# Kernel optimization log

Measured on AMD Instinct MI355X. Metric: run time of the kernel, lower is better.

## Reference

```python
import jax, jax.numpy as jnp
import numpy as np

B, H, W = 8, 128, 128
WIDTH, MODES = 32, 12
NL = 6


def _spectral_conv(x, w):
    # x: [B,C,H,W] real; w: [2, Cin, Cout, m, m, 2] (real/imag packed)
    b, c, h, ww = x.shape
    m = w.shape[3]
    xf = jnp.fft.rfft2(x)  # [B,C,H,W//2+1] complex
    w1 = w[0, ..., 0] + 1j * w[0, ..., 1]
    w2 = w[1, ..., 0] + 1j * w[1, ..., 1]
    top = jnp.einsum('bixy,ioxy->boxy', xf[:, :, :m, :m], w1)
    bot = jnp.einsum('bixy,ioxy->boxy', xf[:, :, -m:, :m], w2)
    out = jnp.zeros((b, w.shape[2], h, ww // 2 + 1), dtype=xf.dtype)
    out = out.at[:, :, :m, :m].set(top).at[:, :, -m:, :m].set(bot)
    return jnp.fft.irfft2(out, s=(h, ww))


def _conv1x1(x, wgt, bia):
    # x: [B,C,H,W], wgt: [O,C], bia: [O]
    return jnp.einsum('bchw,oc->bohw', x, wgt) + bia[None, :, None, None]


def _gelu(x):
    return jax.nn.gelu(x, approximate=False)


def setup_inputs() -> dict:
    key = jax.random.key(0)
    ks = jax.random.split(key, 20)
    scale = 1.0 / (WIDTH * WIDTH)
    d = {}
    d['x'] = jax.random.normal(ks[0], (B, H, W, 4), jnp.float32)
    d['fc0_W'] = jax.random.normal(ks[1], (4, WIDTH), jnp.float32) * 0.5
    d['fc0_b'] = jnp.zeros((WIDTH,), jnp.float32)
    d['spec_w'] = scale * jax.random.uniform(ks[2], (NL, 2, WIDTH, WIDTH, MODES, MODES, 2), jnp.float32)
    d['wW'] = jax.random.normal(ks[3], (NL, WIDTH, WIDTH), jnp.float32) * (1.0 / np.sqrt(WIDTH))
    d['wb'] = jnp.zeros((NL, WIDTH), jnp.float32)
    d['bW'] = jax.random.normal(ks[4], (NL, WIDTH, 2), jnp.float32) * 0.7
    d['bb'] = jnp.zeros((NL, WIDTH), jnp.float32)
    d['cW'] = jax.random.normal(ks[5], (NL, WIDTH, 3), jnp.float32) * 0.57
    d['cb'] = jnp.zeros((NL, WIDTH), jnp.float32)
    d['fc1_W'] = jax.random.normal(ks[6], (WIDTH, 256), jnp.float32) * (1.0 / np.sqrt(WIDTH))
    d['fc1_b'] = jnp.zeros((256,), jnp.float32)
    d['fc3_W'] = jax.random.normal(ks[7], (256, 128), jnp.float32) * (1.0 / 16.0)
    d['fc3_b'] = jnp.zeros((128,), jnp.float32)
    d['fc4_W'] = jax.random.normal(ks[8], (128, 128), jnp.float32) * (1.0 / np.sqrt(128.0))
    d['fc4_b'] = jnp.zeros((128,), jnp.float32)
    d['fc5_W'] = jax.random.normal(ks[9], (128, 1), jnp.float32) * (1.0 / np.sqrt(128.0))
    d['fc5_b'] = jnp.zeros((1,), jnp.float32)
    return d


def reference(x, fc0_W, fc0_b, spec_w, wW, wb, bW, bb, cW, cb,
              fc1_W, fc1_b, fc3_W, fc3_b, fc4_W, fc4_b, fc5_W, fc5_b):
    b, h, w, _ = x.shape
    grid_mesh = jnp.transpose(x[:, :, :, 1:4], (0, 3, 1, 2))  # [B,3,H,W]
    y = x @ fc0_W + fc0_b                                     # [B,H,W,width]
    y = jnp.transpose(y, (0, 3, 1, 2))                        # [B,width,H,W]
    gx = jnp.linspace(0.0, 1.0, h, dtype=jnp.float32)
    gy = jnp.linspace(0.0, 1.0, w, dtype=jnp.float32)
    grid = jnp.stack([
        jnp.broadcast_to(gx[:, None], (h, w)),
        jnp.broadcast_to(gy[None, :], (h, w)),
    ], axis=0)                                                # [2,H,W]
    grid = jnp.broadcast_to(grid[None], (b, 2, h, w))
    for l in range(NL):
        y = _gelu(_spectral_conv(y, spec_w[l])
                  + _conv1x1(y, wW[l], wb[l])
                  + _conv1x1(grid, bW[l], bb[l])
                  + _conv1x1(grid_mesh, cW[l], cb[l]))
    y = jnp.transpose(y, (0, 2, 3, 1))                        # [B,H,W,width]
    y = _gelu(y @ fc1_W + fc1_b)
    y = _gelu(y @ fc3_W + fc3_b)
    y = y @ fc4_W + fc4_b
    y = y @ fc5_W + fc5_b
    return y
```

## Files before the change

### kernel.cpp

```cpp
#include <hip/hip_runtime.h>
#include <math.h>


#define NL 6

typedef unsigned short u16;
typedef __attribute__((ext_vector_type(8))) short short8v;
typedef __attribute__((ext_vector_type(8))) unsigned short ushort8v;
typedef __attribute__((ext_vector_type(4))) unsigned short ushort4v;
typedef __attribute__((ext_vector_type(4))) float f32x4;

__device__ __forceinline__ float gelu_f(float x){
  float z  = x*0.70710678118654752f;
  float az = fabsf(z);
  float t  = __builtin_amdgcn_rcpf(fmaf(0.3275911f, az, 1.0f));
  float p  = t*(0.254829592f + t*(-0.284496736f + t*(1.421413741f +
             t*(-1.453152027f + t*1.061405429f))));
  float e  = __expf(-z*z);
  float er = copysignf(fmaf(-p, e, 1.0f), z);
  return 0.5f*x*(1.0f + er);
}
__device__ __forceinline__ u16 f2bf(float x){
  unsigned u = __float_as_uint(x);
  u += 0x7FFF + ((u>>16)&1);
  return (u16)(u>>16);
}
__device__ __forceinline__ float bf2f(u16 h){
  return __uint_as_float(((unsigned)h)<<16);
}
__device__ __forceinline__ void split2(float v, u16 &hh, u16 &ll){
  unsigned u = __float_as_uint(v);
  hh = (u16)(u>>16);
  float lo = v - __uint_as_float(u & 0xFFFF0000u);
  ll = (u16)(__float_as_uint(lo)>>16);
}

__global__ __launch_bounds__(256) void k_fc0f(const float* __restrict__ x,
                      const float* __restrict__ W, const float* __restrict__ b,
                      float* __restrict__ y, float* __restrict__ F1){
  __shared__ float Ws[128];
  __shared__ float bs[32];
  __shared__ float ys2[2][32][132];
  int t = threadIdx.x;
  if (t < 128) Ws[t] = W[t];
  if (t < 32)  bs[t] = b[t];
  __syncthreads();
  int pix = blockIdx.x*256 + t;
  float4 xv = *reinterpret_cast<const float4*>(x + (size_t)pix*4);
  int bb = pix >> 14, hw = pix & 16383;
  int r = t>>7, w = t&127;
  float* yp = y + (size_t)bb*32*16384 + hw;
  #pragma unroll
  for (int c=0;c<32;c++){
    float acc = bs[c] + xv.x*Ws[c] + xv.y*Ws[32+c] + xv.z*Ws[64+c] + xv.w*Ws[96+c];
    yp[(size_t)c*16384] = acc;
    ys2[r][c][w] = acc;
  }
  __syncthreads();
  int c2 = t>>3, wq = t&7;
  float stc[12], sts[12];
  #pragma unroll
  for (int k=0;k<12;k++){ float s,c; sincospif(k*(1.0f/64.0f), &s, &c); stc[k]=c; sts[k]=s; }
  int gr0 = blockIdx.x*2;
  #pragma unroll
  for (int r2=0;r2<2;r2++){
    float cr[12], ci[12], aR[12], aI[12];
    #pragma unroll
    for (int k=0;k<12;k++){
      float s,c; sincospif((float)(k*wq)*0.25f, &s, &c);
      cr[k]=c; ci[k]=s; aR[k]=0.f; aI[k]=0.f;
    }
    const float* rowp = &ys2[r2][c2][wq*16];
    #pragma unroll
    for (int q=0;q<4;q++){
      float4 xq = *reinterpret_cast<const float4*>(rowp + q*4);
      float xa[4]={xq.x,xq.y,xq.z,xq.w};
      #pragma unroll
      for (int e=0;e<4;e++){
        float xw = xa[e];
        #pragma unroll
        for (int k=0;k<12;k++){
          aR[k] += xw*cr[k];
          aI[k] -= xw*ci[k];
          float nc = cr[k]*stc[k] - ci[k]*sts[k];
          ci[k]    = cr[k]*sts[k] + ci[k]*stc[k];
          cr[k] = nc;
        }
      }
    }
    #pragma unroll
    for (int k=0;k<12;k++){
      aR[k] += __shfl_xor(aR[k],1); aR[k] += __shfl_xor(aR[k],2); aR[k] += __shfl_xor(aR[k],4);
      aI[k] += __shfl_xor(aI[k],1); aI[k] += __shfl_xor(aI[k],2); aI[k] += __shfl_xor(aI[k],4);
    }
    if (wq==0){
      int g = gr0 + r2; int b2 = g>>7, h2 = g&127;
      float* dst = F1 + ((size_t)(b2*32+c2)*128 + h2)*24;
      #pragma unroll
      for (int k=0;k<12;k++){ dst[2*k] = aR[k]; dst[2*k+1] = aI[k]; }
    }
  }
}

__global__ __launch_bounds__(256) void k_wtrans(const float* __restrict__ w, float* __restrict__ wT){
  __shared__ float buf[16][32][25];
  int t=threadIdx.x;
  int beta = blockIdx.x;
  int l = beta/48, r = beta%48;
  int hf = r/24; int r2 = r%24;
  int kym = r2>>1; int i0 = (r2&1)*16;
  const float* src = w + (size_t)l*589824 + (size_t)hf*294912 + kym*24;
  float* dst = wT + (size_t)l*589824 + (size_t)hf*294912 + (size_t)kym*24576;
  for (int j=t; j<12288; j+=256){
    int i = j/768, rem = j%768, o = rem/24, kxri = rem%24;
    buf[i][o][kxri] = src[(size_t)(i0+i)*9216 + o*288 + kxri];
  }
  __syncthreads();
  for (int j=t; j<12288; j+=256){
    int kx = j>>10, rem = j&1023, i = rem>>6, orr = rem&63, o = orr>>1, ri = orr&1;
    dst[(size_t)kx*2048 + o*64 + (i0+i)*2 + ri] = buf[i][o][kx*2+ri];
  }
}

__global__ __launch_bounds__(256) void k_wprep(const float* __restrict__ W1, const float* __restrict__ W3,
                       const float* __restrict__ W4,
                       const float* __restrict__ b4, const float* __restrict__ w5,
                       const float* __restrict__ b5,
                       u16* __restrict__ W1h, u16* __restrict__ W1l,
                       u16* __restrict__ W3h, u16* __restrict__ W3l,
                       u16* __restrict__ W4h, u16* __restrict__ W4l,
                       u16* __restrict__ Emh, u16* __restrict__ Eml,
                       u16* __restrict__ E2h, u16* __restrict__ E2l,
                       u16* __restrict__ E3h, u16* __restrict__ E3l,
                       float* __restrict__ c45){
  __shared__ float buf[32][132];
  int t = threadIdx.x, bid = blockIdx.x;
  if (bid < 8){
    int k0 = bid*32;
    for (int i=t;i<4096;i+=256){ int k=i>>7, n=i&127; buf[k][n] = W3[(size_t)(k0+k)*128 + n]; }
    __syncthreads();
    int n = t>>1, kq = t&1;
    #pragma unroll
    for (int kk=0;kk<16;kk++){
      int k = kq*16 + kk;
      float v = buf[k][n];
      u16 hh = f2bf(v);
      W3h[(size_t)bid*4096 + n*32 + k] = hh;
      W3l[(size_t)bid*4096 + n*32 + k] = f2bf(v - bf2f(hh));
    }
  } else if (bid == 8){
    __shared__ float red[256];
    int n = t;
    #pragma unroll
    for (int c=0;c<32;c++){
      float v = W1[(size_t)c*256 + n];
      u16 hh = f2bf(v);
      W1h[n*32 + c] = hh;
      W1l[n*32 + c] = f2bf(v - bf2f(hh));
    }
    red[t] = (t<128)? b4[t]*w5[t] : 0.f;
    __syncthreads();
    for (int s2=128; s2>0; s2>>=1){
      if (t<s2) red[t] += red[t+s2];
      __syncthreads();
    }
    if (t==0) c45[0] = red[0] + b5[0];
  } else if (bid <= 12){
    int k0 = (bid-9)*32;
    for (int i=t;i<4096;i+=256){ int k=i>>7, n=i&127; buf[k][n] = W4[(size_t)(k0+k)*128 + n]; }
    __syncthreads();
    int n = t>>1, kq = t&1;
    #pragma unroll
    for (int kk=0;kk<16;kk++){
      int k = kq*16 + kk;
      float v = buf[k][n];
      u16 hh = f2bf(v);
      W4h[(size_t)(bid-9)*4096 + n*32 + k] = hh;
      W4l[(size_t)(bid-9)*4096 + n*32 + k] = f2bf(v - bf2f(hh));
    }
  } else if (bid == 13){
    for (int i=t;i<4096;i+=256){
      int m=i>>7, w=i&127;
      float v=0.f;
      if (m<24){ float s,c; sincospif((float)((m>>1)*w)*(1.0f/64.0f), &s, &c); v = (m&1)? -s : c; }
      u16 hh, ll; split2(v, hh, ll);
      Emh[i]=hh; Eml[i]=ll;
    }
  } else if (bid == 14){
    for (int i=t;i<12288;i+=256){
      int m=i>>8, k=i&255;
      int kyi = (m<24)? m : m-24;
      int ky  = (kyi<12)? kyi : kyi+104;
      int h   = k&127;
      int mm  = (ky*h)&127;
      float s,c; sincospif((float)mm*(1.0f/64.0f), &s, &c);
      bool sinSlot = k>=128;
      float v;
      if (m<24) v = sinSlot? s : c;
      else      v = sinSlot? c : -s;
      u16 hh, ll; split2(v, hh, ll);
      E2h[i]=hh; E2l[i]=ll;
    }
  } else {
    for (int i=t;i<8192;i+=256){
      int h=i>>6, k=i&63;
      float v=0.f;
      if (k<48){
        int kyi = (k<24)? k : k-24;
        int ky  = (kyi<12)? kyi : kyi+104;
        int mm  = (ky*h)&127;
        float s,c; sincospif((float)mm*(1.0f/64.0f), &s, &c);
        v = ((k<24)? c : s) * (1.0f/16384.0f);
      }
      u16 hh, ll; split2(v, hh, ll);
      E3h[i]=hh; E3l[i]=ll;
    }
  }
}

__global__ __launch_bounds__(256) void k_dfth(const float* __restrict__ F1,
                      const u16* __restrict__ E2h, const u16* __restrict__ E2l,
                      float* __restrict__ F2){
  __shared__ u16 Fth[16*264], Ftl[16*264];
  int t=threadIdx.x;
  int bc = blockIdx.x;
  int b = bc>>5, c = bc&31;
  const float* src = F1 + (size_t)bc*3072;
  for (int i=t;i<3072;i+=256){
    int h = i/24, col = i - h*24;
    int kx = col>>1, ri = col&1;
    u16 hh, ll; split2(src[i], hh, ll);
    int idx = kx*264 + ri*128 + h;
    Fth[idx] = hh; Ftl[idx] = ll;
  }
  __syncthreads();
  int wv = t>>6, lane = t&63, lr = lane&15, lg = lane>>4;
  if (wv < 3){
    f32x4 acc = (f32x4){0.f,0.f,0.f,0.f};
    #pragma unroll
    for (int ks=0; ks<8; ++ks){
      short8v af = *reinterpret_cast<const short8v*>(E2h + (size_t)(wv*16+lr)*256 + ks*32 + lg*8);
      short8v ag = *reinterpret_cast<const short8v*>(E2l + (size_t)(wv*16+lr)*256 + ks*32 + lg*8);
      short8v bf = *reinterpret_cast<const short8v*>(&Fth[lr*264 + ks*32 + lg*8]);
      short8v bg = *reinterpret_cast<const short8v*>(&Ftl[lr*264 + ks*32 + lg*8]);
      acc = __builtin_amdgcn_mfma_f32_16x16x32_bf16(af, bf, acc, 0,0,0);
      acc = __builtin_amdgcn_mfma_f32_16x16x32_bf16(af, bg, acc, 0,0,0);
      acc = __builtin_amdgcn_mfma_f32_16x16x32_bf16(ag, bf, acc, 0,0,0);
    }
    if (lr < 12){
      #pragma unroll
      for (int r=0;r<4;r++){
        int m = wv*16 + 4*lg + r;
        int kyi = (m<24)? m : m-24;
        int ri  = (m<24)? 0 : 1;
        F2[(((size_t)b*24 + kyi)*24 + 2*lr + ri)*32 + c] = acc[r];
      }
    }
  }
}

__global__ __launch_bounds__(576) void k_mixid(const float* __restrict__ F2, const float* __restrict__ wTl,
                      const u16* __restrict__ E3h, const u16* __restrict__ E3l,
                      float* __restrict__ S1){
  __shared__ u16 Bh[32*72], Bl[32*72];
  int t=threadIdx.x;
  int bo = blockIdx.x;
  int b = bo>>5, o = bo&31;
  for (int i=t; i<24*24; i+=576){
    int row = i/24, k = 48 + i - (i/24)*24;
    Bh[row*72 + k] = 0; Bl[row*72 + k] = 0;
  }
  {
    int pair = t>>1, half = t&1;
    int kx = pair%12, kyi = pair/12;
    int hf = kyi<12?0:1, kym = kyi<12?kyi:kyi-12;
    const float* fpr = F2 + (((size_t)b*24 + kyi)*24 + 2*kx)*32 + half*16;
    const float* fpi = fpr + 32;
    const float* wp = wTl + (size_t)(hf*12+kym)*24576 + kx*2048 + o*64 + half*32;
    float gr=0.f, gi=0.f;
    #pragma unroll 8
    for (int i=0;i<16;i++){
      float2 wv = *reinterpret_cast<const float2*>(wp + 2*i);
      float ar = fpr[i], ai = fpi[i];
      gr += ar*wv.x - ai*wv.y;
      gi += ar*wv.y + ai*wv.x;
    }
    gr += __shfl_xor(gr,1);
    gi += __shfl_xor(gi,1);
    if (half==0){
      u16 grh, grl, gih, gil, nih, nil;
      split2(gr, grh, grl);
      split2(gi, gih, gil);
      split2(-gi, nih, nil);
      int r0 = (2*kx)*72, r1 = (2*kx+1)*72;
      Bh[r0 + kyi]      = grh; Bl[r0 + kyi]      = grl;
      Bh[r0 + 24 + kyi] = nih; Bl[r0 + 24 + kyi] = nil;
      Bh[r1 + kyi]      = gih; Bl[r1 + kyi]      = gil;
      Bh[r1 + 24 + kyi] = grh; Bl[r1 + 24 + kyi] = grl;
    }
  }
  __syncthreads();
  int wv = t>>6, lane = t&63, lr = lane&15, lg = lane>>4;
  if (wv < 8){
    f32x4 acc[2];
    acc[0] = (f32x4){0.f,0.f,0.f,0.f};
    acc[1] = (f32x4){0.f,0.f,0.f,0.f};
    #pragma unroll
    for (int ks=0; ks<2; ++ks){
      short8v af = *reinterpret_cast<const short8v*>(E3h + (size_t)(wv*16+lr)*64 + ks*32 + lg*8);
      short8v ag = *reinterpret_cast<const short8v*>(E3l + (size_t)(wv*16+lr)*64 + ks*32 + lg*8);
      #pragma unroll
      for (int nt=0; nt<2; ++nt){
        short8v bf = *reinterpret_cast<const short8v*>(&Bh[(nt*16+lr)*72 + ks*32 + lg*8]);
        short8v bg = *reinterpret_cast<const short8v*>(&Bl[(nt*16+lr)*72 + ks*32 + lg*8]);
        acc[nt] = __builtin_amdgcn_mfma_f32_16x16x32_bf16(af, bf, acc[nt], 0,0,0);
        acc[nt] = __builtin_amdgcn_mfma_f32_16x16x32_bf16(af, bg, acc[nt], 0,0,0);
        acc[nt] = __builtin_amdgcn_mfma_f32_16x16x32_bf16(ag, bf, acc[nt], 0,0,0);
      }
    }
    float* dst = S1 + (size_t)bo*3072;
    #pragma unroll
    for (int nt=0; nt<2; ++nt){
      int n = nt*16 + lr;
      if (n < 24){
        #pragma unroll
        for (int r=0;r<4;r++){
          int h = wv*16 + 4*lg + r;
          dst[h*24 + n] = acc[nt][r];
        }
      }
    }
  }
}

template<int LAST>
__global__ __launch_bounds__(512) void k_combine2(const float* __restrict__ yin, const float* __restrict__ S1,
                         const float* __restrict__ x,
                         const float* __restrict__ wWl, const float* __restrict__ wbl,
                         const float* __restrict__ bWl, const float* __restrict__ bbl,
                         const float* __restrict__ cWl, const float* __restrict__ cbl,
                         const u16* __restrict__ Emh, const u16* __restrict__ Eml,
                         float* __restrict__ yout, float* __restrict__ F1,
                         u16* __restrict__ yb16){
  __shared__ float ysT[128][33];
  __shared__ u16 ybsp[2][32][136];
  int t=threadIdx.x;
  int b = blockIdx.x>>7, h = blockIdx.x&127;
  for (int i=t;i<4096;i+=512){ int c=i>>7, w=i&127;
    ysT[w][c] = yin[(((size_t)(b*32+c))*128+h)*128+w]; }
  __syncthreads();
  int w = t&127;
  int og = __builtin_amdgcn_readfirstlane(t>>7);
  float ct[12], st[12];
  ct[0]=1.f; st[0]=0.f;
  float c1,s1v; sincospif(w*(1.0f/64.0f), &s1v, &c1);
  #pragma unroll
  for (int k=0;k<11;k++){ ct[k+1] = ct[k]*c1 - st[k]*s1v; st[k+1] = ct[k]*s1v + st[k]*c1; }
  float gx = h*(1.0f/127.0f), gy = w*(1.0f/127.0f);
  float4 xm = *reinterpret_cast<const float4*>(x + (((size_t)(b*128+h))*128+w)*4);
  float m1=xm.y, m2=xm.z, m3=xm.w;
  const float* wo  = wWl + og*256;
  const float* s1o = S1 + (size_t)b*98304 + (size_t)og*8*3072 + h*24;
  float accv[8];
  #pragma unroll
  for (int oi=0;oi<8;oi++){
    int o = og*8+oi;
    float bse = wbl[o] + bbl[o] + cbl[o] + gx*bWl[o*2] + gy*bWl[o*2+1]
              + m1*cWl[o*3] + m2*cWl[o*3+1] + m3*cWl[o*3+2];
    const float* sp = s1o + (size_t)oi*3072;
    float spec = sp[0];
    #pragma unroll
    for (int kx=1;kx<12;kx++) spec += 2.0f*(sp[2*kx]*ct[kx] - sp[2*kx+1]*st[kx]);
    accv[oi] = bse + spec;
  }
  #pragma unroll
  for (int c=0;c<32;c++){
    float xc = ysT[w][c];
    #pragma unroll
    for (int oi=0;oi<8;oi++) accv[oi] += wo[oi*32+c]*xc;
  }
  #pragma unroll
  for (int oi=0;oi<8;oi++){
    float g = gelu_f(accv[oi]);
    int o = og*8+oi;
    if constexpr (!LAST){
      u16 hh, ll; split2(g, hh, ll);
      ybsp[0][o][w] = hh;
      ybsp[1][o][w] = ll;
      yout[(((size_t)(b*32+o))*128+h)*128+w] = g;
    } else {
      ybsp[0][o][w] = f2bf(g);
    }
  }
  __syncthreads();
  if constexpr (!LAST){
    int wv = t>>6;
    if (wv < 4){
      int lane = t&63, lr = lane&15, lg = lane>>4;
      int mt = wv&1, oj = wv>>1;
      f32x4 acc = (f32x4){0.f,0.f,0.f,0.f};
      #pragma unroll
      for (int ks=0; ks<4; ++ks){
        short8v ef = *reinterpret_cast<const short8v*>(Emh + (size_t)(mt*16+lr)*128 + ks*32 + lg*8);
        short8v eg = *reinterpret_cast<const short8v*>(Eml + (size_t)(mt*16+lr)*128 + ks*32 + lg*8);
        short8v yf = *reinterpret_cast<const short8v*>(&ybsp[0][oj*16+lr][ks*32+lg*8]);
        short8v yg = *reinterpret_cast<const short8v*>(&ybsp[1][oj*16+lr][ks*32+lg*8]);
        acc = __builtin_amdgcn_mfma_f32_16x16x32_bf16(ef, yf, acc, 0,0,0);
        acc = __builtin_amdgcn_mfma_f32_16x16x32_bf16(ef, yg, acc, 0,0,0);
        acc = __builtin_amdgcn_mfma_f32_16x16x32_bf16(eg, yf, acc, 0,0,0);
      }
      if (mt==0 || lg<2){
        int m = mt*16 + 4*lg;
        int o = oj*16 + lr;
        float4 v; v.x=acc[0]; v.y=acc[1]; v.z=acc[2]; v.w=acc[3];
        *reinterpret_cast<float4*>(&F1[((size_t)(b*32+o)*128 + h)*24 + m]) = v;
      }
    }
  } else {
    int wr = t>>2, hf4 = t&3;
    size_t pix = (size_t)b*16384 + h*128 + wr;
    ushort8v h8;
    #pragma unroll
    for (int q=0;q<8;q++) h8[q] = ybsp[0][hf4*8 + q][wr];
    *reinterpret_cast<ushort8v*>(yb16 + pix*32 + hf4*8) = h8;
  }
}

__global__ __launch_bounds__(256) void k_headm(
    const u16* __restrict__ Yb,
    const u16* __restrict__ W1h, const u16* __restrict__ W1l,
    const float* __restrict__ b1,
    const u16* __restrict__ W3h, const u16* __restrict__ W3l,
    const float* __restrict__ b3,
    const u16* __restrict__ W4h, const u16* __restrict__ W4l,
    const float* __restrict__ c45, const float* __restrict__ w5,
    float* __restrict__ out){
  __shared__ u16 Ac[64*264];
  __shared__ float b1s[256];
  __shared__ float b3s[128], w5s[128];
  __shared__ float part2[2][64];
  int t = threadIdx.x;
  int wv = t>>6, lane = t&63, lr = lane&15, lg = lane>>4;
  int P0 = blockIdx.x*64;
  b1s[t] = b1[t];
  if (t<128){ b3s[t]=b3[t]; w5s[t]=w5[t]; }
  int wn3 = wv>>1, wp = wv&1;
  short8v yb;
  {
    size_t p = (size_t)P0 + wv*16 + lr;
    yb = *reinterpret_cast<const short8v*>(Yb + p*32 + lg*8);
  }
  __syncthreads();

  unsigned q[8][2][2];
  #pragma unroll
  for (int kt=0; kt<8; ++kt){
    f32x4 a1[2];
    a1[0]=(f32x4){0,0,0,0}; a1[1]=(f32x4){0,0,0,0};
    #pragma unroll
    for (int i=0;i<2;i++){
      int n1 = kt*32 + i*16 + lr;
      short8v w1f = *reinterpret_cast<const short8v*>(W1h + (size_t)n1*32 + lg*8);
      short8v w1g = *reinterpret_cast<const short8v*>(W1l + (size_t)n1*32 + lg*8);
      a1[i] = __builtin_amdgcn_mfma_f32_16x16x32_bf16(w1f, yb, a1[i], 0,0,0);
      a1[i] = __builtin_amdgcn_mfma_f32_16x16x32_bf16(w1g, yb, a1[i], 0,0,0);
    }
    #pragma unroll
    for (int i=0;i<2;i++){
      int n1b = kt*32 + i*16 + 4*lg;
      u16 v0 = f2bf(gelu_f(a1[i][0] + b1s[n1b+0]));
      u16 v1 = f2bf(gelu_f(a1[i][1] + b1s[n1b+1]));
      u16 v2 = f2bf(gelu_f(a1[i][2] + b1s[n1b+2]));
      u16 v3 = f2bf(gelu_f(a1[i][3] + b1s[n1b+3]));
      q[kt][i][0] = (unsigned)v0 | ((unsigned)v1<<16);
      q[kt][i][1] = (unsigned)v2 | ((unsigned)v3<<16);
    }
  }
  {
    int p = wv*16 + lr;
    #pragma unroll
    for (int kt=0; kt<8; ++kt){
      #pragma unroll
      for (int i=0;i<2;i++){
        union { unsigned u[2]; ushort4v s; } cv;
        cv.u[0] = q[kt][i][0]; cv.u[1] = q[kt][i][1];
        *reinterpret_cast<ushort4v*>(&Ac[p*264 + kt*32 + i*16 + 4*lg]) = cv.s;
      }
    }
  }
  __syncthreads();
  f32x4 acc3[4][2];
  #pragma unroll
  for (int i=0;i<4;i++){ acc3[i][0]=(f32x4){0,0,0,0}; acc3[i][1]=(f32x4){0,0,0,0}; }
  #pragma unroll
  for (int kt=0; kt<8; ++kt){
    short8v ab[2];
    #pragma unroll
    for (int j=0;j<2;j++){
      int pb = wp*32 + j*16 + lr;
      ab[j] = *reinterpret_cast<const short8v*>(&Ac[pb*264 + kt*32 + lg*8]);
    }
    #pragma unroll
    for (int i=0;i<4;i++){
      int n3 = wn3*64 + i*16 + lr;
      short8v w3f = *reinterpret_cast<const short8v*>(W3h + (size_t)kt*4096 + n3*32 + lg*8);
      short8v w3g = *reinterpret_cast<const short8v*>(W3l + (size_t)kt*4096 + n3*32 + lg*8);
      #pragma unroll
      for (int j=0;j<2;j++){
        acc3[i][j] = __builtin_amdgcn_mfma_f32_16x16x32_bf16(w3f, ab[j], acc3[i][j], 0,0,0);
        acc3[i][j] = __builtin_amdgcn_mfma_f32_16x16x32_bf16(w3g, ab[j], acc3[i][j], 0,0,0);
      }
    }
  }
  __syncthreads();
  u16* A2 = Ac;
  #pragma unroll
  for (int i=0;i<4;i++){
    int n3b = wn3*64 + i*16 + 4*lg;
    #pragma unroll
    for (int j=0;j<2;j++){
      int p = wp*32 + j*16 + lr;
      ushort4v hv;
      #pragma unroll
      for (int r=0;r<4;r++){
        hv[r] = f2bf(gelu_f(acc3[i][j][r] + b3s[n3b+r]));
      }
      *reinterpret_cast<ushort4v*>(&A2[p*136 + n3b]) = hv;
    }
  }
  __syncthreads();
  f32x4 acc4[4][2];
  #pragma unroll
  for (int i=0;i<4;i++){ acc4[i][0]=(f32x4){0,0,0,0}; acc4[i][1]=(f32x4){0,0,0,0}; }
  #pragma unroll
  for (int ks=0; ks<4; ++ks){
    short8v p2[2];
    #pragma unroll
    for (int j=0;j<2;j++){
      int p = wp*32 + j*16 + lr;
      p2[j] = *reinterpret_cast<const short8v*>(&A2[p*136 + ks*32 + lg*8]);
    }
    #pragma unroll
    for (int i2=0;i2<4;i2++){
      int n4 = wn3*64 + i2*16 + lr;
      short8v w4f = *reinterpret_cast<const short8v*>(W4h + (size_t)ks*4096 + n4*32 + lg*8);
      short8v w4g = *reinterpret_cast<const short8v*>(W4l + (size_t)ks*4096 + n4*32 + lg*8);
      #pragma unroll
      for (int j=0;j<2;j++){
        acc4[i2][j] = __builtin_amdgcn_mfma_f32_16x16x32_bf16(w4f, p2[j], acc4[i2][j], 0,0,0);
        acc4[i2][j] = __builtin_amdgcn_mfma_f32_16x16x32_bf16(w4g, p2[j], acc4[i2][j], 0,0,0);
      }
    }
  }
  #pragma unroll
  for (int j=0;j<2;j++){
    float part = 0.f;
    #pragma unroll
    for (int i2=0;i2<4;i2++){
      #pragma unroll
      for (int r=0;r<4;r++){
        int n4 = wn3*64 + i2*16 + 4*lg + r;
        part += acc4[i2][j][r] * w5s[n4];
      }
    }
    part += __shfl_xor(part, 16); part += __shfl_xor(part, 32);
    if (lg==0) part2[wn3][wp*32 + j*16 + lr] = part;
  }
  __syncthreads();
  if (t<64) out[P0 + t] = part2[0][t] + part2[1][t] + c45[0];
}

extern "C" void kernel_launch(void* const* d_in, const int* in_sizes, int n_in,
                              void* d_out, int out_size, void* d_ws, size_t ws_size,
                              hipStream_t stream){
  const float* x     = (const float*)d_in[0];
  const float* fc0_W = (const float*)d_in[1];
  const float* fc0_b = (const float*)d_in[2];
  const float* spec_w= (const float*)d_in[3];
  const float* wW    = (const float*)d_in[4];
  const float* wb    = (const float*)d_in[5];
  const float* bW    = (const float*)d_in[6];
  const float* bb    = (const float*)d_in[7];
  const float* cW    = (const float*)d_in[8];
  const float* cb    = (const float*)d_in[9];
  const float* fc1_W = (const float*)d_in[10];
  const float* fc1_b = (const float*)d_in[11];
  const float* fc3_W = (const float*)d_in[12];
  const float* fc3_b = (const float*)d_in[13];
  const float* fc4_W = (const float*)d_in[14];
  const float* fc4_b = (const float*)d_in[15];
  const float* fc5_W = (const float*)d_in[16];
  const float* fc5_b = (const float*)d_in[17];
  float* out = (float*)d_out;
  float* ws  = (float*)d_ws;

  float* y_a = ws;
  float* y_b = y_a + 4194304;
  float* wT  = y_b + 4194304;
  float* F2  = wT + 3538944;
  float* S1  = F2 + 147456;
  float* F1  = S1 + 786432;
  float* WP  = F1 + 786432;
  u16*   W1h = (u16*)WP;
  u16*   W1l = W1h + 8192;
  u16*   W3h = W1l + 8192;
  u16*   W3l = W3h + 32768;
  u16*   W4h = W3l + 32768;
  u16*   W4l = W4h + 16384;
  u16*   Emh = W4l + 16384;
  u16*   Eml = Emh + 4096;
  u16*   E2h = Eml + 4096;
  u16*   E2l = E2h + 12288;
  u16*   E3h = E2l + 12288;
  u16*   E3l = E3h + 8192;
  float* c45 = (float*)(E3l + 8192);
  u16*   Yb16 = (u16*)y_a;

  k_fc0f<<<512,256,0,stream>>>(x, fc0_W, fc0_b, y_a, F1);
  k_wtrans<<<288,256,0,stream>>>(spec_w, wT);
  k_wprep<<<16,256,0,stream>>>(fc1_W, fc3_W, fc4_W, fc4_b, fc5_W, fc5_b,
                               W1h, W1l, W3h, W3l, W4h, W4l, Emh, Eml,
                               E2h, E2l, E3h, E3l, c45);

  for (int l=0;l<NL;l++){
    float* yin  = (l&1)? y_b : y_a;
    float* yout = (l&1)? y_a : y_b;
    k_dfth<<<256,256,0,stream>>>(F1, E2h, E2l, F2);
    k_mixid<<<256,576,0,stream>>>(F2, wT + (size_t)l*589824, E3h, E3l, S1);
    if (l < NL-1){
      k_combine2<0><<<1024,512,0,stream>>>(yin, S1, x,
                                     wW + (size_t)l*1024, wb + (size_t)l*32,
                                     bW + (size_t)l*64,  bb + (size_t)l*32,
                                     cW + (size_t)l*96,  cb + (size_t)l*32,
                                     Emh, Eml,
                                     yout, F1, nullptr);
    } else {
      k_combine2<1><<<1024,512,0,stream>>>(yin, S1, x,
                                     wW + (size_t)l*1024, wb + (size_t)l*32,
                                     bW + (size_t)l*64,  bb + (size_t)l*32,
                                     cW + (size_t)l*96,  cb + (size_t)l*32,
                                     Emh, Eml,
                                     nullptr, nullptr, Yb16);
    }
  }

  k_headm<<<2048,256,0,stream>>>(Yb16, W1h, W1l, fc1_b, W3h, W3l, fc3_b,
                                 W4h, W4l, c45, fc5_W, out);
}
```

Before: 328.2 us.

## Move combine step to MFMA with split-bf16 channel-last activations

The activation buffer changes from fp32 NCHW to channel-last hi/lo bf16 pairs. The combine kernel now does the 1x1 channel mix and the inverse W-direction DFT as split-bf16 MFMA matmuls, using a precomputed twiddle matrix E4 and pre-split weights and biases, instead of scalar FMA loops with a transpose through shared memory. The spectral intermediate S1 is also stored as hi/lo bf16. The aim is to cut scalar ALU work and global traffic per layer. The cost is a 3-term split-bf16 approximation of fp32 and more prep work in k_wprep.

```diff
diff --git a/kernel.cpp b/kernel.cpp
--- a/kernel.cpp
+++ b/kernel.cpp
@@ -37,7 +37,8 @@
 
 __global__ __launch_bounds__(256) void k_fc0f(const float* __restrict__ x,
                       const float* __restrict__ W, const float* __restrict__ b,
-                      float* __restrict__ y, float* __restrict__ F1){
+                      u16* __restrict__ Ybh, u16* __restrict__ Ybl,
+                      float* __restrict__ F1){
   __shared__ float Ws[128];
   __shared__ float bs[32];
   __shared__ float ys2[2][32][132];
@@ -47,14 +48,23 @@
   __syncthreads();
   int pix = blockIdx.x*256 + t;
   float4 xv = *reinterpret_cast<const float4*>(x + (size_t)pix*4);
-  int bb = pix >> 14, hw = pix & 16383;
   int r = t>>7, w = t&127;
-  float* yp = y + (size_t)bb*32*16384 + hw;
+  ushort8v hv[4], lv[4];
   #pragma unroll
   for (int c=0;c<32;c++){
     float acc = bs[c] + xv.x*Ws[c] + xv.y*Ws[32+c] + xv.z*Ws[64+c] + xv.w*Ws[96+c];
-    yp[(size_t)c*16384] = acc;
     ys2[r][c][w] = acc;
+    u16 hh, ll; split2(acc, hh, ll);
+    hv[c>>3][c&7] = hh; lv[c>>3][c&7] = ll;
+  }
+  {
+    u16* dh = Ybh + (size_t)pix*32;
+    u16* dl = Ybl + (size_t)pix*32;
+    #pragma unroll
+    for (int q=0;q<4;q++){
+      *reinterpret_cast<ushort8v*>(dh + q*8) = hv[q];
+      *reinterpret_cast<ushort8v*>(dl + q*8) = lv[q];
+    }
   }
   __syncthreads();
   int c2 = t>>3, wq = t&7;
@@ -126,13 +136,17 @@
                        const float* __restrict__ W4,
                        const float* __restrict__ b4, const float* __restrict__ w5,
                        const float* __restrict__ b5,
+                       const float* __restrict__ wW, const float* __restrict__ wb,
+                       const float* __restrict__ bb, const float* __restrict__ cb,
                        u16* __restrict__ W1h, u16* __restrict__ W1l,
                        u16* __restrict__ W3h, u16* __restrict__ W3l,
                        u16* __restrict__ W4h, u16* __restrict__ W4l,
                        u16* __restrict__ Emh, u16* __restrict__ Eml,
                        u16* __restrict__ E2h, u16* __restrict__ E2l,
                        u16* __restrict__ E3h, u16* __restrict__ E3l,
-                       float* __restrict__ c45){
+                       u16* __restrict__ Wch, u16* __restrict__ Wcl,
+                       u16* __restrict__ E4h, u16* __restrict__ E4l,
+                       float* __restrict__ bsum, float* __restrict__ c45){
   __shared__ float buf[32][132];
   int t = threadIdx.x, bid = blockIdx.x;
   if (bid < 8){
@@ -201,7 +215,7 @@
       u16 hh, ll; split2(v, hh, ll);
       E2h[i]=hh; E2l[i]=ll;
     }
-  } else {
+  } else if (bid == 15){
     for (int i=t;i<8192;i+=256){
       int h=i>>6, k=i&63;
       float v=0.f;
@@ -214,6 +228,28 @@
       }
       u16 hh, ll; split2(v, hh, ll);
       E3h[i]=hh; E3l[i]=ll;
+    }
+  } else if (bid == 16){
+    for (int i=t;i<6144;i+=256){
+      float v = wW[i];
+      u16 hh, ll; split2(v, hh, ll);
+      Wch[i]=hh; Wcl[i]=ll;
+    }
+    if (t < 192) bsum[t] = wb[t] + bb[t] + cb[t];
+  } else {
+    for (int i=t;i<4096;i+=256){
+      int w=i>>5, k=i&31;
+      float v=0.f;
+      if (k < 24){
+        int kx = k>>1, ri = k&1;
+        if (kx==0) v = ri? 0.f : 1.f;
+        else {
+          float s,c; sincospif((float)(kx*w)*(1.0f/64.0f), &s, &c);
+          v = ri? -2.f*s : 2.f*c;
+        }
+      }
+      u16 hh, ll; split2(v, hh, ll);
+      E4h[i]=hh; E4l[i]=ll;
     }
   }
 }
@@ -261,7 +297,7 @@
 
 __global__ __launch_bounds__(576) void k_mixid(const float* __restrict__ F2, const float* __restrict__ wTl,
                       const u16* __restrict__ E3h, const u16* __restrict__ E3l,
-                      float* __restrict__ S1){
+                      u16* __restrict__ S1h, u16* __restrict__ S1l){
   __shared__ u16 Bh[32*72], Bl[32*72];
   int t=threadIdx.x;
   int bo = blockIdx.x;
@@ -318,7 +354,6 @@
         acc[nt] = __builtin_amdgcn_mfma_f32_16x16x32_bf16(ag, bf, acc[nt], 0,0,0);
       }
     }
-    float* dst = S1 + (size_t)bo*3072;
     #pragma unroll
     for (int nt=0; nt<2; ++nt){
       int n = nt*16 + lr;
@@ -326,7 +361,9 @@
         #pragma unroll
         for (int r=0;r<4;r++){
           int h = wv*16 + 4*lg + r;
-          dst[h*24 + n] = acc[nt][r];
+          size_t off = (size_t)bo*3072 + h*24 + n;
+          u16 hh, ll; split2(acc[nt][r], hh, ll);
+          S1h[off] = hh; S1l[off] = ll;
         }
       }
     }
@@ -334,95 +371,105 @@
 }
 
 template<int LAST>
-__global__ __launch_bounds__(512) void k_combine2(const float* __restrict__ yin, const float* __restrict__ S1,
-                         const float* __restrict__ x,
-                         const float* __restrict__ wWl, const float* __restrict__ wbl,
-                         const float* __restrict__ bWl, const float* __restrict__ bbl,
-                         const float* __restrict__ cWl, const float* __restrict__ cbl,
-                         const u16* __restrict__ Emh, const u16* __restrict__ Eml,
-                         float* __restrict__ yout, float* __restrict__ F1,
-                         u16* __restrict__ yb16){
-  __shared__ float ysT[128][33];
+__global__ __launch_bounds__(256) void k_combine3(
+    const u16* __restrict__ Ybh_in, const u16* __restrict__ Ybl_in,
+    const u16* __restrict__ S1h, const u16* __restrict__ S1l,
+    const float* __restrict__ x,
+    const u16* __restrict__ Wch, const u16* __restrict__ Wcl,
+    const u16* __restrict__ E4h, const u16* __restrict__ E4l,
+    const float* __restrict__ bsuml,
+    const float* __restrict__ bWl, const float* __restrict__ cWl,
+    const u16* __restrict__ Emh, const u16* __restrict__ Eml,
+    float* __restrict__ F1,
+    u16* __restrict__ Ybh_out, u16* __restrict__ Ybl_out){
   __shared__ u16 ybsp[2][32][136];
+  __shared__ float bs[32], bwS[64], cwS[96];
   int t=threadIdx.x;
   int b = blockIdx.x>>7, h = blockIdx.x&127;
-  for (int i=t;i<4096;i+=512){ int c=i>>7, w=i&127;
-    ysT[w][c] = yin[(((size_t)(b*32+c))*128+h)*128+w]; }
-  __syncthreads();
-  int w = t&127;
-  int og = __builtin_amdgcn_readfirstlane(t>>7);
-  float ct[12], st[12];
-  ct[0]=1.f; st[0]=0.f;
-  float c1,s1v; sincospif(w*(1.0f/64.0f), &s1v, &c1);
-  #pragma unroll
-  for (int k=0;k<11;k++){ ct[k+1] = ct[k]*c1 - st[k]*s1v; st[k+1] = ct[k]*s1v + st[k]*c1; }
-  float gx = h*(1.0f/127.0f), gy = w*(1.0f/127.0f);
-  float4 xm = *reinterpret_cast<const float4*>(x + (((size_t)(b*128+h))*128+w)*4);
-  float m1=xm.y, m2=xm.z, m3=xm.w;
-  const float* wo  = wWl + og*256;
-  const float* s1o = S1 + (size_t)b*98304 + (size_t)og*8*3072 + h*24;
-  float accv[8];
-  #pragma unroll
-  for (int oi=0;oi<8;oi++){
-    int o = og*8+oi;
-    float bse = wbl[o] + bbl[o] + cbl[o] + gx*bWl[o*2] + gy*bWl[o*2+1]
-              + m1*cWl[o*3] + m2*cWl[o*3+1] + m3*cWl[o*3+2];
-    const float* sp = s1o + (size_t)oi*3072;
-    float spec = sp[0];
-    #pragma unroll
-    for (int kx=1;kx<12;kx++) spec += 2.0f*(sp[2*kx]*ct[kx] - sp[2*kx+1]*st[kx]);
-    accv[oi] = bse + spec;
-  }
-  #pragma unroll
-  for (int c=0;c<32;c++){
-    float xc = ysT[w][c];
-    #pragma unroll
-    for (int oi=0;oi<8;oi++) accv[oi] += wo[oi*32+c]*xc;
-  }
-  #pragma unroll
-  for (int oi=0;oi<8;oi++){
-    float g = gelu_f(accv[oi]);
-    int o = og*8+oi;
-    if constexpr (!LAST){
-      u16 hh, ll; split2(g, hh, ll);
-      ybsp[0][o][w] = hh;
-      ybsp[1][o][w] = ll;
-      yout[(((size_t)(b*32+o))*128+h)*128+w] = g;
-    } else {
-      ybsp[0][o][w] = f2bf(g);
-    }
-  }
-  __syncthreads();
-  if constexpr (!LAST){
-    int wv = t>>6;
-    if (wv < 4){
-      int lane = t&63, lr = lane&15, lg = lane>>4;
-      int mt = wv&1, oj = wv>>1;
-      f32x4 acc = (f32x4){0.f,0.f,0.f,0.f};
-      #pragma unroll
-      for (int ks=0; ks<4; ++ks){
-        short8v ef = *reinterpret_cast<const short8v*>(Emh + (size_t)(mt*16+lr)*128 + ks*32 + lg*8);
-        short8v eg = *reinterpret_cast<const short8v*>(Eml + (size_t)(mt*16+lr)*128 + ks*32 + lg*8);
-        short8v yf = *reinterpret_cast<const short8v*>(&ybsp[0][oj*16+lr][ks*32+lg*8]);
-        short8v yg = *reinterpret_cast<const short8v*>(&ybsp[1][oj*16+lr][ks*32+lg*8]);
-        acc = __builtin_amdgcn_mfma_f32_16x16x32_bf16(ef, yf, acc, 0,0,0);
-        acc = __builtin_amdgcn_mfma_f32_16x16x32_bf16(ef, yg, acc, 0,0,0);
-        acc = __builtin_amdgcn_mfma_f32_16x16x32_bf16(eg, yf, acc, 0,0,0);
-      }
-      if (mt==0 || lg<2){
-        int m = mt*16 + 4*lg;
-        int o = oj*16 + lr;
-        float4 v; v.x=acc[0]; v.y=acc[1]; v.z=acc[2]; v.w=acc[3];
-        *reinterpret_cast<float4*>(&F1[((size_t)(b*32+o)*128 + h)*24 + m]) = v;
-      }
-    }
-  } else {
-    int wr = t>>2, hf4 = t&3;
-    size_t pix = (size_t)b*16384 + h*128 + wr;
-    ushort8v h8;
-    #pragma unroll
-    for (int q=0;q<8;q++) h8[q] = ybsp[0][hf4*8 + q][wr];
-    *reinterpret_cast<ushort8v*>(yb16 + pix*32 + hf4*8) = h8;
+  if (t<32) bs[t]=bsuml[t];
+  else if (t>=64 && t<128) bwS[t-64]=bWl[t-64];
+  else if (t>=128 && t<224) cwS[t-128]=cWl[t-128];
+  __syncthreads();
+  int wv=t>>6, lane=t&63, lr=lane&15, lg=lane>>4;
+  f32x4 acc[2][2];
+  #pragma unroll
+  for (int ot=0;ot<2;++ot){ acc[ot][0]=(f32x4){0,0,0,0}; acc[ot][1]=(f32x4){0,0,0,0}; }
+  #pragma unroll
+  for (int ot=0; ot<2; ++ot){
+    int o = ot*16+lr;
+    short8v af = *reinterpret_cast<const short8v*>(Wch + o*32 + lg*8);
+    short8v al = *reinterpret_cast<const short8v*>(Wcl + o*32 + lg*8);
+    #pragma unroll
+    for (int j=0;j<2;++j){
+      int w = (2*wv+j)*16 + lr;
+      size_t yoff = (((size_t)(b*128+h))*128 + w)*32 + lg*8;
+      short8v bh = *reinterpret_cast<const short8v*>(Ybh_in + yoff);
+      short8v bl = *reinterpret_cast<const short8v*>(Ybl_in + yoff);
+      acc[ot][j] = __builtin_amdgcn_mfma_f32_16x16x32_bf16(af, bh, acc[ot][j], 0,0,0);
+      acc[ot][j] = __builtin_amdgcn_mfma_f32_16x16x32_bf16(af, bl, acc[ot][j], 0,0,0);
+      acc[ot][j] = __builtin_amdgcn_mfma_f32_16x16x32_bf16(al, bh, acc[ot][j], 0,0,0);
+    }
+  }
+  #pragma unroll
+  for (int ot=0; ot<2; ++ot){
+    int o = ot*16+lr;
+    size_t soff = (((size_t)(b*32+o))*128 + h)*24 + lg*8;
+    short8v ah = *reinterpret_cast<const short8v*>(S1h + soff);
+    short8v al2 = *reinterpret_cast<const short8v*>(S1l + soff);
+    #pragma unroll
+    for (int j=0;j<2;++j){
+      int w = (2*wv+j)*16 + lr;
+      short8v eh = *reinterpret_cast<const short8v*>(E4h + w*32 + lg*8);
+      short8v el = *reinterpret_cast<const short8v*>(E4l + w*32 + lg*8);
+      acc[ot][j] = __builtin_amdgcn_mfma_f32_16x16x32_bf16(ah, eh, acc[ot][j], 0,0,0);
+      acc[ot][j] = __builtin_amdgcn_mfma_f32_16x16x32_bf16(al2, eh, acc[ot][j], 0,0,0);
+      acc[ot][j] = __builtin_amdgcn_mfma_f32_16x16x32_bf16(ah, el, acc[ot][j], 0,0,0);
+    }
+  }
+  float gx = h*(1.0f/127.0f);
+  #pragma unroll
+  for (int j=0;j<2;++j){
+    int w = (2*wv+j)*16 + lr;
+    float4 xm = *reinterpret_cast<const float4*>(x + (((size_t)(b*128+h))*128+w)*4);
+    float gy = w*(1.0f/127.0f);
+    #pragma unroll
+    for (int ot=0;ot<2;++ot){
+      ushort4v hv, lvv;
+      #pragma unroll
+      for (int r=0;r<4;++r){
+        int o = ot*16 + 4*lg + r;
+        float v = acc[ot][j][r] + bs[o] + gx*bwS[2*o] + gy*bwS[2*o+1]
+                + xm.y*cwS[3*o] + xm.z*cwS[3*o+1] + xm.w*cwS[3*o+2];
+        float g = gelu_f(v);
+        u16 hh, ll; split2(g, hh, ll);
+        hv[r]=hh; lvv[r]=ll;
+        if constexpr(!LAST){ ybsp[0][o][w]=hh; ybsp[1][o][w]=ll; }
+      }
+      size_t base = (((size_t)(b*128+h))*128 + w)*32 + ot*16 + 4*lg;
+      *reinterpret_cast<ushort4v*>(Ybh_out + base) = hv;
+      *reinterpret_cast<ushort4v*>(Ybl_out + base) = lvv;
+    }
+  }
+  if constexpr(!LAST){
+    __syncthreads();
+    int mt = wv&1, oj = wv>>1;
+    f32x4 accm = (f32x4){0.f,0.f,0.f,0.f};
+    #pragma unroll
+    for (int ks=0; ks<4; ++ks){
+      short8v ef = *reinterpret_cast<const short8v*>(Emh + (size_t)(mt*16+lr)*128 + ks*32 + lg*8);
+      short8v eg = *reinterpret_cast<const short8v*>(Eml + (size_t)(mt*16+lr)*128 + ks*32 + lg*8);
+      short8v yf = *reinterpret_cast<const short8v*>(&ybsp[0][oj*16+lr][ks*32+lg*8]);
+      short8v yg = *reinterpret_cast<const short8v*>(&ybsp[1][oj*16+lr][ks*32+lg*8]);
+      accm = __builtin_amdgcn_mfma_f32_16x16x32_bf16(ef, yf, accm, 0,0,0);
+      accm = __builtin_amdgcn_mfma_f32_16x16x32_bf16(ef, yg, accm, 0,0,0);
+      accm = __builtin_amdgcn_mfma_f32_16x16x32_bf16(eg, yf, accm, 0,0,0);
+    }
+    if (mt==0 || lg<2){
+      int m = mt*16 + 4*lg;
+      int o = oj*16 + lr;
+      float4 v; v.x=accm[0]; v.y=accm[1]; v.z=accm[2]; v.w=accm[3];
+      *reinterpret_cast<float4*>(&F1[((size_t)(b*32+o)*128 + h)*24 + m]) = v;
+    }
   }
 }
 
@@ -451,7 +498,6 @@
     yb = *reinterpret_cast<const short8v*>(Yb + p*32 + lg*8);
   }
   __syncthreads();
-
   unsigned q[8][2][2];
   #pragma unroll
   for (int kt=0; kt<8; ++kt){
@@ -594,13 +640,14 @@
   float* out = (float*)d_out;
   float* ws  = (float*)d_ws;
 
-  float* y_a = ws;
-  float* y_b = y_a + 4194304;
-  float* wT  = y_b + 4194304;
-  float* F2  = wT + 3538944;
-  float* S1  = F2 + 147456;
-  float* F1  = S1 + 786432;
-  float* WP  = F1 + 786432;
+  u16*   YbA  = (u16*)ws;
+  u16*   YbB  = YbA + 8388608;
+  float* wT   = ws + 8388608;
+  float* F2   = wT + 3538944;
+  u16*   S1h  = (u16*)(F2 + 147456);
+  u16*   S1l  = S1h + 786496;
+  float* F1   = (float*)(S1l + 786496);
+  float* WP   = F1 + 786432;
   u16*   W1h = (u16*)WP;
   u16*   W1l = W1h + 8192;
   u16*   W3h = W1l + 8192;
@@ -613,37 +660,45 @@
   u16*   E2l = E2h + 12288;
   u16*   E3h = E2l + 12288;
   u16*   E3l = E3h + 8192;
-  float* c45 = (float*)(E3l + 8192);
-  u16*   Yb16 = (u16*)y_a;
-
-  k_fc0f<<<512,256,0,stream>>>(x, fc0_W, fc0_b, y_a, F1);
+  u16*   Wch = E3l + 8192;
+  u16*   Wcl = Wch + 6144;
+  u16*   E4h = Wcl + 6144;
+  u16*   E4l = E4h + 4096;
+  float* bsum = (float*)(E4l + 4096);
+  float* c45  = bsum + 192;
+  u16*   YbhA = YbA;
+  u16*   YblA = YbA + 4194304;
+  u16*   YbhB = YbB;
+  u16*   YblB = YbB + 4194304;
+
+  k_fc0f<<<512,256,0,stream>>>(x, fc0_W, fc0_b, YbhA, YblA, F1);
   k_wtrans<<<288,256,0,stream>>>(spec_w, wT);
-  k_wprep<<<16,256,0,stream>>>(fc1_W, fc3_W, fc4_W, fc4_b, fc5_W, fc5_b,
+  k_wprep<<<18,256,0,stream>>>(fc1_W, fc3_W, fc4_W, fc4_b, fc5_W, fc5_b,
+                               wW, wb, bb, cb,
                                W1h, W1l, W3h, W3l, W4h, W4l, Emh, Eml,
-                               E2h, E2l, E3h, E3l, c45);
+                               E2h, E2l, E3h, E3l, Wch, Wcl, E4h, E4l,
+                               bsum, c45);
 
   for (int l=0;l<NL;l++){
-    float* yin  = (l&1)? y_b : y_a;
-    float* yout = (l&1)? y_a : y_b;
+    const u16* Yih = (l&1)? YbhB : YbhA;
+    const u16* Yil = (l&1)? YblB : YblA;
+    u16* Yoh = (l&1)? YbhA : YbhB;
+    u16* Yol = (l&1)? YblA : YblB;
     k_dfth<<<256,256,0,stream>>>(F1, E2h, E2l, F2);
-    k_mixid<<<256,576,0,stream>>>(F2, wT + (size_t)l*589824, E3h, E3l, S1);
+    k_mixid<<<256,576,0,stream>>>(F2, wT + (size_t)l*589824, E3h, E3l, S1h, S1l);
     if (l < NL-1){
-      k_combine2<0><<<1024,512,0,stream>>>(yin, S1, x,
-                                     wW + (size_t)l*1024, wb + (size_t)l*32,
-                                     bW + (size_t)l*64,  bb + (size_t)l*32,
-                                     cW + (size_t)l*96,  cb + (size_t)l*32,
-                                     Emh, Eml,
-                                     yout, F1, nullptr);
+      k_combine3<0><<<1024,256,0,stream>>>(Yih, Yil, S1h, S1l, x,
+                                     Wch + l*1024, Wcl + l*1024, E4h, E4l,
+                                     bsum + l*32, bW + (size_t)l*64, cW + (size_t)l*96,
+                                     Emh, Eml, F1, Yoh, Yol);
     } else {
-      k_combine2<1><<<1024,512,0,stream>>>(yin, S1, x,
-                                     wW + (size_t)l*1024, wb + (size_t)l*32,
-                                     bW + (size_t)l*64,  bb + (size_t)l*32,
-                                     cW + (size_t)l*96,  cb + (size_t)l*32,
-                                     Emh, Eml,
-                                     nullptr, nullptr, Yb16);
-    }
-  }
-
-  k_headm<<<2048,256,0,stream>>>(Yb16, W1h, W1l, fc1_b, W3h, W3l, fc3_b,
+      k_combine3<1><<<1024,256,0,stream>>>(Yih, Yil, S1h, S1l, x,
+                                     Wch + l*1024, Wcl + l*1024, E4h, E4l,
+                                     bsum + l*32, bW + (size_t)l*64, cW + (size_t)l*96,
+                                     Emh, Eml, nullptr, Yoh, Yol);
+    }
+  }
+
+  k_headm<<<2048,256,0,stream>>>(YbhA, W1h, W1l, fc1_b, W3h, W3l, fc3_b,
                                  W4h, W4l, c45, fc5_W, out);
 }
```

Measured after the change: 315.0 us (median of 2 runs). 4.0% less time.
